# Kernel optimization log

Measured on AMD Instinct MI355X. Metric: run time of the kernel, lower is better.

Reference implementation:

```python
import jax, jax.numpy as jnp
import numpy as np

N, E, DIN, H, D = 100000, 1600000, 256, 4, 32  # nodes, edges, in_feats, heads, out_feats
NEG_SLOPE = 0.2


def setup_inputs() -> dict:
    key = jax.random.key(0)
    ks = jax.random.split(key, 6)
    feat = jax.random.normal(ks[0], (N, DIN), jnp.float32)
    src = jax.random.randint(ks[1], (E,), 0, N, jnp.int32)
    dst = jax.random.randint(ks[2], (E,), 0, N, jnp.int32)
    # fc weight, xavier-normal-ish scale
    W = jax.random.normal(ks[3], (H * D, DIN), jnp.float32) * (2.0 / (DIN + H * D)) ** 0.5
    attn_l = jax.random.normal(ks[4], (1, H, D), jnp.float32) * 0.1
    attn_r = jax.random.normal(ks[5], (1, H, D), jnp.float32) * 0.1
    bias = jnp.zeros((H * D,), jnp.float32)
    return dict(feat=feat, src=src, dst=dst, W=W, attn_l=attn_l, attn_r=attn_r, bias=bias)


def reference(feat, src, dst, W, attn_l, attn_r, bias):
    n = feat.shape[0]
    # node projection: [N, H, D]
    ft = (feat @ W.T).reshape(n, H, D)
    # per-node attention logits: [N, H]
    el = jnp.sum(ft * attn_l, axis=-1)
    er = jnp.sum(ft * attn_r, axis=-1)
    # edge scores (u_add_v + LeakyReLU): [E, H]
    e = jax.nn.leaky_relu(el[src] + er[dst], NEG_SLOPE)
    # segment softmax over incoming edges of each dst node
    m = jax.ops.segment_max(e, dst, num_segments=n)
    m = jnp.where(jnp.isfinite(m), m, 0.0)  # guard zero-in-degree nodes
    ae = jnp.exp(e - m[dst])
    denom = jax.ops.segment_sum(ae, dst, num_segments=n)
    a = ae / denom[dst]  # [E, H]
    # weighted scatter-aggregate (u_mul_e + sum): [N, H, D]
    out = jax.ops.segment_sum(ft[src] * a[:, :, None], dst, num_segments=n)
    return out + bias.reshape(1, H, D)
```

## Files before the change

### kernel.cpp

```cpp
#include <hip/hip_runtime.h>
#include <hip/hip_bf16.h>


#define DIN 256
#define HD 128
#define NEG_SLOPE 0.2f
#define BUCKW 1024
#define BINE 4096
#define CAP  18432

typedef float f32x4 __attribute__((ext_vector_type(4)));
typedef short s16x8 __attribute__((ext_vector_type(8)));

static __device__ __forceinline__ unsigned short f2bf(float x) {
    unsigned u = __float_as_uint(x);
    unsigned r = (u + 0x7FFFu + ((u >> 16) & 1u)) >> 16;
    return (unsigned short)r;
}
static __device__ __forceinline__ uint pk2(float a, float b) {
    return (uint)f2bf(a) | ((uint)f2bf(b) << 16);
}

__global__ __launch_bounds__(512, 4) void gemm_bin_kernel(
    const float* __restrict__ feat, const float* __restrict__ W,
    unsigned short* __restrict__ ftu, const float* __restrict__ attn_l,
    const float* __restrict__ attn_r, float* __restrict__ el,
    float* __restrict__ er, int n,
    const int* __restrict__ src, const int* __restrict__ dst,
    int* __restrict__ gcur, int* __restrict__ esrc,
    unsigned short* __restrict__ edlo, int e, int ngb)
{
    __shared__ unsigned short Bs[32768];
    const int tid = threadIdx.x;

    if ((int)blockIdx.x >= ngb) {
        int* h  = (int*)Bs;
        int* lb = h + 128;
        int* gb = lb + 128;
        int* sc = gb + 128;
        int* ptot = sc + 128;
        int* ps = ptot + 4;
        unsigned short* pd = (unsigned short*)(ps + BINE);
        unsigned char*  pb = (unsigned char*)(pd + BINE);
        if (tid < 128) h[tid] = 0;
        __syncthreads();
        const int base = ((int)blockIdx.x - ngb) * BINE + tid * 8;
        int sv[8], dv[8], rk[8];
        const int cnt = min(8, max(0, e - base));
        if (cnt == 8) {
            *(int4*)&sv[0] = *(const int4*)&src[base];
            *(int4*)&sv[4] = *(const int4*)&src[base + 4];
            *(int4*)&dv[0] = *(const int4*)&dst[base];
            *(int4*)&dv[4] = *(const int4*)&dst[base + 4];
        } else {
            for (int m = 0; m < cnt; ++m) { sv[m] = src[base + m]; dv[m] = dst[base + m]; }
        }
        for (int m = 0; m < cnt; ++m)
            rk[m] = atomicAdd(&h[dv[m] >> 10], 1);
        __syncthreads();
        if (tid < 128) sc[tid] = h[tid];
        __syncthreads();
        for (int off = 1; off < 128; off <<= 1) {
            int v = (tid < 128 && tid >= off) ? sc[tid - off] : 0;
            __syncthreads();
            if (tid < 128) sc[tid] += v;
            __syncthreads();
        }
        if (tid < 128) {
            lb[tid] = sc[tid] - h[tid];
            if (h[tid] > 0) gb[tid] = atomicAdd(&gcur[tid], h[tid]);
        }
        if (tid == 127) *ptot = sc[127];
        __syncthreads();
        for (int m = 0; m < cnt; ++m) {
            int b = dv[m] >> 10;
            int pos = lb[b] + rk[m];
            ps[pos] = sv[m];
            pd[pos] = (unsigned short)(dv[m] & 1023);
            pb[pos] = (unsigned char)b;
        }
        __syncthreads();
        const int tot = *ptot;
        for (int s = tid; s < tot; s += 512) {
            int b = pb[s];
            int o = b * CAP + gb[b] + (s - lb[b]);
            esrc[o] = ps[s];
            edlo[o] = pd[s];
        }
        return;
    }

    const int lane = tid & 63;
    const int wv = tid >> 6;
    const int l16 = lane & 15, lq = lane >> 4;
    const int row0 = (int)blockIdx.x * 256 + wv * 32;

#pragma unroll
    for (int it = 0; it < 8; ++it) {
        const int cell = it * 512 + tid;
        const int kb = cell >> 7, c = cell & 127;
        const float4* wp = (const float4*)&W[(size_t)c * DIN + kb * 8];
        float4 f0 = wp[0], f1 = wp[1];
        uint4 pk;
        pk.x = pk2(f0.x, f0.y); pk.y = pk2(f0.z, f0.w);
        pk.z = pk2(f1.x, f1.y); pk.w = pk2(f1.z, f1.w);
        *(uint4*)&Bs[(size_t)cell * 8] = pk;
    }
    __syncthreads();

    f32x4 acc[2][8] = {};
    const int ar0 = row0 + l16, ar1 = row0 + 16 + l16;
    const bool ok0 = ar0 < n, ok1 = ar1 < n;
    const float* fp0 = feat + (size_t)ar0 * DIN;
    const float* fp1 = feat + (size_t)ar1 * DIN;
#pragma unroll
    for (int kc = 0; kc < 4; ++kc) {
#pragma unroll
        for (int kk = 0; kk < 2; ++kk) {
            const int koff = kc * 64 + kk * 32 + lq * 8;
            union { s16x8 v; uint w[4]; } a0, a1;
            a0.v = (s16x8)(short)0;
            a1.v = (s16x8)(short)0;
            if (ok0) {
                float4 fa = *(const float4*)(fp0 + koff);
                float4 fb = *(const float4*)(fp0 + koff + 4);
                a0.w[0] = pk2(fa.x, fa.y); a0.w[1] = pk2(fa.z, fa.w);
                a0.w[2] = pk2(fb.x, fb.y); a0.w[3] = pk2(fb.z, fb.w);
            }
            if (ok1) {
                float4 fa = *(const float4*)(fp1 + koff);
                float4 fb = *(const float4*)(fp1 + koff + 4);
                a1.w[0] = pk2(fa.x, fa.y); a1.w[1] = pk2(fa.z, fa.w);
                a1.w[2] = pk2(fb.x, fb.y); a1.w[3] = pk2(fb.z, fb.w);
            }
            const int kb = kc * 8 + kk * 4 + lq;
#pragma unroll
            for (int n4 = 0; n4 < 8; ++n4) {
                s16x8 b = *(const s16x8*)&Bs[(kb * 128 + n4 * 16 + l16) * 8];
                acc[0][n4] = __builtin_amdgcn_mfma_f32_16x16x32_bf16(a0.v, b, acc[0][n4], 0, 0, 0);
                acc[1][n4] = __builtin_amdgcn_mfma_f32_16x16x32_bf16(a1.v, b, acc[1][n4], 0, 0, 0);
            }
        }
    }

    float al8[8], ar8[8];
#pragma unroll
    for (int n4 = 0; n4 < 8; ++n4) {
        al8[n4] = attn_l[n4 * 16 + l16];
        ar8[n4] = attn_r[n4 * 16 + l16];
    }
#pragma unroll
    for (int m = 0; m < 2; ++m) {
#pragma unroll
        for (int n4 = 0; n4 < 8; ++n4)
#pragma unroll
            for (int j = 0; j < 4; ++j) {
                int r = row0 + m * 16 + lq * 4 + j;
                if (r < n) ftu[(size_t)r * HD + n4 * 16 + l16] = f2bf(acc[m][n4][j]);
            }
#pragma unroll
        for (int j = 0; j < 4; ++j) {
            const int r = row0 + m * 16 + lq * 4 + j;
#pragma unroll
            for (int h = 0; h < 4; ++h) {
                float sl = acc[m][2 * h][j] * al8[2 * h] + acc[m][2 * h + 1][j] * al8[2 * h + 1];
                float sr = acc[m][2 * h][j] * ar8[2 * h] + acc[m][2 * h + 1][j] * ar8[2 * h + 1];
#pragma unroll
                for (int off = 1; off < 16; off <<= 1) {
                    sl += __shfl_xor(sl, off);
                    sr += __shfl_xor(sr, off);
                }
                if (l16 == ((j << 2) | h) && r < n) {
                    el[r * 4 + h] = sl;
                    er[r * 4 + h] = sr;
                }
            }
        }
    }
}

__global__ __launch_bounds__(1024) void fine_kernel(
    const int* __restrict__ esrc, const unsigned short* __restrict__ edlo,
    const int* __restrict__ gcur, int* __restrict__ beg, int* __restrict__ endp,
    int* __restrict__ srcs_sorted, int n)
{
    __shared__ int deg[1024];
    __shared__ int wsum[16];
    const int b = blockIdx.x, tid = threadIdx.x;
    const int lane = tid & 63, wid = tid >> 6;
    const int lo = b * CAP;
    const int cnt = gcur[b];
    const int nbase = b << 10;
    deg[tid] = 0;
    __syncthreads();
    for (int i = tid; i < cnt; i += 1024)
        atomicAdd(&deg[edlo[lo + i]], 1);
    __syncthreads();
    const int d = deg[tid];
    int x = d;
#pragma unroll
    for (int off = 1; off < 64; off <<= 1) {
        int y = __shfl(x, lane - off);
        if (lane >= off) x += y;
    }
    if (lane == 63) wsum[wid] = x;
    __syncthreads();
    if (tid == 0) {
        int run = 0;
#pragma unroll
        for (int i2 = 0; i2 < 16; ++i2) { int t2 = wsum[i2]; wsum[i2] = run; run += t2; }
    }
    __syncthreads();
    const int start = lo + wsum[wid] + x - d;
    if (nbase + tid < n) {
        beg[nbase + tid] = start;
        endp[nbase + tid] = start + d;
    }
    deg[tid] = start;
    __syncthreads();
    for (int i = tid; i < cnt; i += 1024) {
        int dd = edlo[lo + i];
        int pos = atomicAdd(&deg[dd], 1);
        srcs_sorted[pos] = esrc[lo + i];
    }
}

__global__ __launch_bounds__(256) void aggregate_kernel(
    const unsigned short* __restrict__ ftu, const float* __restrict__ el,
    const float* __restrict__ er, const int* __restrict__ beg,
    const int* __restrict__ endp, const int* __restrict__ srcs,
    const float* __restrict__ bias, float* __restrict__ out, int n)
{
    __shared__ float plds[4][64][4];
    int v = (int)((blockIdx.x * (unsigned)blockDim.x + threadIdx.x) >> 6);
    if (v >= n) return;
    const int wv = (threadIdx.x >> 6) & 3;
    const int lane = threadIdx.x & 63;
    const int h = lane >> 4;
    const int beg_ = beg[v], end_ = endp[v];
    const float4 er4 = *(const float4*)(er + (size_t)v * 4);
    const uint* __restrict__ ftu32 = (const uint*)ftu;
    float* pl = &plds[wv][0][0];
    float dn = 0.f;
    float acc0 = 0.f, acc1 = 0.f;
    for (int t = beg_; t < end_; t += 64) {
        const int cnt = min(64, end_ - t);
        int sj = 0;
        float p0 = 0.f, p1 = 0.f, p2 = 0.f, p3 = 0.f;
        if (lane < cnt) {
            sj = srcs[t + lane];
            float4 elv = *(const float4*)(el + (size_t)sj * 4);
            float e0 = elv.x + er4.x, e1 = elv.y + er4.y;
            float e2 = elv.z + er4.z, e3 = elv.w + er4.w;
            e0 = fmaxf(e0, NEG_SLOPE * e0);
            e1 = fmaxf(e1, NEG_SLOPE * e1);
            e2 = fmaxf(e2, NEG_SLOPE * e2);
            e3 = fmaxf(e3, NEG_SLOPE * e3);
            p0 = __expf(e0); p1 = __expf(e1);
            p2 = __expf(e2); p3 = __expf(e3);
        }
        *(float4*)&pl[lane << 2] = make_float4(p0, p1, p2, p3);
        __builtin_amdgcn_wave_barrier();
        for (int j = 0; j < cnt; j += 16) {
            uint u[16];
            float pj[16];
#pragma unroll
            for (int m = 0; m < 16; ++m) {
                int sjb = __shfl(sj, j + m);
                u[m] = ftu32[(uint)sjb * 64u + (uint)lane];
                pj[m] = pl[((j + m) << 2) + h];
            }
#pragma unroll
            for (int m = 0; m < 16; ++m) {
                dn += pj[m];
                acc0 = fmaf(pj[m], __uint_as_float(u[m] << 16), acc0);
                acc1 = fmaf(pj[m], __uint_as_float(u[m] & 0xffff0000u), acc1);
            }
        }
        __builtin_amdgcn_wave_barrier();
    }
    float inv = dn > 0.f ? 1.f / dn : 0.f;
    float b0 = bias[lane << 1], b1 = bias[(lane << 1) + 1];
    float2 o = make_float2(fmaf(acc0, inv, b0), fmaf(acc1, inv, b1));
    *(float2*)&out[(size_t)v * HD + (lane << 1)] = o;
}

extern "C" void kernel_launch(void* const* d_in, const int* in_sizes, int n_in,
                              void* d_out, int out_size, void* d_ws, size_t ws_size,
                              hipStream_t stream) {
    const float* feat   = (const float*)d_in[0];
    const int*   src    = (const int*)d_in[1];
    const int*   dst    = (const int*)d_in[2];
    const float* W      = (const float*)d_in[3];
    const float* attn_l = (const float*)d_in[4];
    const float* attn_r = (const float*)d_in[5];
    const float* bias   = (const float*)d_in[6];
    float* out = (float*)d_out;
    const int N = in_sizes[0] / DIN;
    const int E = in_sizes[1];
    const int NBUCK = (N + BUCKW - 1) / BUCKW;
    const int NGB = (N + 255) / 256;
    const int EB = (E + BINE - 1) / BINE;

    char* w = (char*)d_ws;
    auto alloc = [&](size_t bytes) {
        char* p = w;
        w += (bytes + 255) & ~(size_t)255;
        return p;
    };
    unsigned short* ftu         = (unsigned short*)alloc((size_t)N * HD * 2);
    float*          el          = (float*)alloc((size_t)N * 4 * 4);
    float*          er          = (float*)alloc((size_t)N * 4 * 4);
    int*            beg         = (int*)alloc((size_t)N * 4);
    int*            endp        = (int*)alloc((size_t)N * 4);
    int*            srcs_sorted = (int*)alloc((size_t)NBUCK * CAP * 4);
    int*            esrc        = (int*)alloc((size_t)NBUCK * CAP * 4);
    unsigned short* edlo        = (unsigned short*)alloc((size_t)NBUCK * CAP * 2);
    int*            gcur        = (int*)alloc(128 * 4);
    (void)ws_size;

    hipMemsetAsync(gcur, 0, 128 * 4, stream);
    gemm_bin_kernel<<<NGB + EB, 512, 0, stream>>>(
        feat, W, ftu, attn_l, attn_r, el, er, N,
        src, dst, gcur, esrc, edlo, E, NGB);
    fine_kernel<<<NBUCK, 1024, 0, stream>>>(esrc, edlo, gcur, beg, endp, srcs_sorted, N);
    aggregate_kernel<<<(N + 3) / 4, 256, 0, stream>>>(ftu, el, er, beg, endp, srcs_sorted, bias, out, N);
}
```

Measured before the change: 144.9 us.

## Retile projection GEMM to 128-row blocks with swizzled LDS A-tiles

The fused GEMM/binning kernel now uses 128-row tiles with a 4x2 wave grid, so each wave computes 32 rows by 64 columns instead of 32 rows by all 128 columns. The feature rows are staged through LDS with an XOR swizzle, and W is loaded in two K-halves, which shrinks the shared-memory footprint from 64KB to 48KB. The intent is to raise occupancy and spread the GEMM over more blocks. The cost is more barriers and extra LDS traffic for A, plus W is now reconverted by twice as many blocks.

```diff
diff --git a/kernel.cpp b/kernel.cpp
--- a/kernel.cpp
+++ b/kernel.cpp
@@ -8,6 +8,7 @@
 #define BUCKW 1024
 #define BINE 4096
 #define CAP  18432
+#define TM   128
 
 typedef float f32x4 __attribute__((ext_vector_type(4)));
 typedef short s16x8 __attribute__((ext_vector_type(8)));
@@ -30,11 +31,11 @@
     int* __restrict__ gcur, int* __restrict__ esrc,
     unsigned short* __restrict__ edlo, int e, int ngb)
 {
-    __shared__ unsigned short Bs[32768];
+    __shared__ unsigned short S[24576];
     const int tid = threadIdx.x;
 
     if ((int)blockIdx.x >= ngb) {
-        int* h  = (int*)Bs;
+        int* h  = (int*)S;
         int* lb = h + 128;
         int* gb = lb + 128;
         int* sc = gb + 128;
@@ -90,89 +91,96 @@
         return;
     }
 
+    unsigned short* Bsh = S;
+    unsigned short* As  = S + 16384;
     const int lane = tid & 63;
     const int wv = tid >> 6;
+    const int wr = wv >> 1, wc = wv & 1;
     const int l16 = lane & 15, lq = lane >> 4;
-    const int row0 = (int)blockIdx.x * 256 + wv * 32;
-
-#pragma unroll
-    for (int it = 0; it < 8; ++it) {
-        const int cell = it * 512 + tid;
-        const int kb = cell >> 7, c = cell & 127;
-        const float4* wp = (const float4*)&W[(size_t)c * DIN + kb * 8];
-        float4 f0 = wp[0], f1 = wp[1];
-        uint4 pk;
-        pk.x = pk2(f0.x, f0.y); pk.y = pk2(f0.z, f0.w);
-        pk.z = pk2(f1.x, f1.y); pk.w = pk2(f1.z, f1.w);
-        *(uint4*)&Bs[(size_t)cell * 8] = pk;
-    }
-    __syncthreads();
-
-    f32x4 acc[2][8] = {};
-    const int ar0 = row0 + l16, ar1 = row0 + 16 + l16;
-    const bool ok0 = ar0 < n, ok1 = ar1 < n;
-    const float* fp0 = feat + (size_t)ar0 * DIN;
-    const float* fp1 = feat + (size_t)ar1 * DIN;
-#pragma unroll
-    for (int kc = 0; kc < 4; ++kc) {
-#pragma unroll
-        for (int kk = 0; kk < 2; ++kk) {
-            const int koff = kc * 64 + kk * 32 + lq * 8;
-            union { s16x8 v; uint w[4]; } a0, a1;
-            a0.v = (s16x8)(short)0;
-            a1.v = (s16x8)(short)0;
-            if (ok0) {
-                float4 fa = *(const float4*)(fp0 + koff);
-                float4 fb = *(const float4*)(fp0 + koff + 4);
-                a0.w[0] = pk2(fa.x, fa.y); a0.w[1] = pk2(fa.z, fa.w);
-                a0.w[2] = pk2(fb.x, fb.y); a0.w[3] = pk2(fb.z, fb.w);
-            }
-            if (ok1) {
-                float4 fa = *(const float4*)(fp1 + koff);
-                float4 fb = *(const float4*)(fp1 + koff + 4);
-                a1.w[0] = pk2(fa.x, fa.y); a1.w[1] = pk2(fa.z, fa.w);
-                a1.w[2] = pk2(fb.x, fb.y); a1.w[3] = pk2(fb.z, fb.w);
-            }
-            const int kb = kc * 8 + kk * 4 + lq;
-#pragma unroll
-            for (int n4 = 0; n4 < 8; ++n4) {
-                s16x8 b = *(const s16x8*)&Bs[(kb * 128 + n4 * 16 + l16) * 8];
-                acc[0][n4] = __builtin_amdgcn_mfma_f32_16x16x32_bf16(a0.v, b, acc[0][n4], 0, 0, 0);
-                acc[1][n4] = __builtin_amdgcn_mfma_f32_16x16x32_bf16(a1.v, b, acc[1][n4], 0, 0, 0);
-            }
-        }
-    }
-
-    float al8[8], ar8[8];
-#pragma unroll
-    for (int n4 = 0; n4 < 8; ++n4) {
-        al8[n4] = attn_l[n4 * 16 + l16];
-        ar8[n4] = attn_r[n4 * 16 + l16];
+    const int row0 = (int)blockIdx.x * TM;
+
+    f32x4 acc[2][4] = {};
+
+    for (int p = 0; p < 2; ++p) {
+#pragma unroll
+        for (int it = 0; it < 4; ++it) {
+            const int cell = it * 512 + tid;
+            const int kbl = cell >> 7, c = cell & 127;
+            const float4* wp = (const float4*)&W[(size_t)c * DIN + (p * 16 + kbl) * 8];
+            float4 f0 = wp[0], f1 = wp[1];
+            uint4 pk;
+            pk.x = pk2(f0.x, f0.y); pk.y = pk2(f0.z, f0.w);
+            pk.z = pk2(f1.x, f1.y); pk.w = pk2(f1.z, f1.w);
+            *(uint4*)&Bsh[(size_t)cell * 8] = pk;
+        }
+#pragma unroll
+        for (int kc2 = 0; kc2 < 2; ++kc2) {
+            const int kc = p * 2 + kc2;
+#pragma unroll
+            for (int it = 0; it < 2; ++it) {
+                const int cell = it * 512 + tid;
+                const int r = cell >> 3, kq8 = (cell & 7) << 3;
+                uint4 pk = make_uint4(0, 0, 0, 0);
+                if (row0 + r < n) {
+                    const float4* ap = (const float4*)&feat[(size_t)(row0 + r) * DIN + kc * 64 + kq8];
+                    float4 f0 = ap[0], f1 = ap[1];
+                    pk.x = pk2(f0.x, f0.y); pk.y = pk2(f0.z, f0.w);
+                    pk.z = pk2(f1.x, f1.y); pk.w = pk2(f1.z, f1.w);
+                }
+                const int sidx = (r * 64 + kq8) ^ ((r & 7) << 3);
+                *(uint4*)&As[sidx] = pk;
+            }
+            __syncthreads();
+            const int ra = wr * 32 + l16;
+            const int swz = (ra & 7) << 3;
+#pragma unroll
+            for (int kk = 0; kk < 2; ++kk) {
+                const int kb8 = kk * 32 + lq * 8;
+                s16x8 a0 = *(const s16x8*)&As[(ra * 64 + kb8) ^ swz];
+                s16x8 a1 = *(const s16x8*)&As[((ra + 16) * 64 + kb8) ^ swz];
+                const int kbl = kc2 * 8 + kk * 4 + lq;
+#pragma unroll
+                for (int n4 = 0; n4 < 4; ++n4) {
+                    s16x8 b = *(const s16x8*)&Bsh[(kbl * 128 + wc * 64 + n4 * 16 + l16) * 8];
+                    acc[0][n4] = __builtin_amdgcn_mfma_f32_16x16x32_bf16(a0, b, acc[0][n4], 0, 0, 0);
+                    acc[1][n4] = __builtin_amdgcn_mfma_f32_16x16x32_bf16(a1, b, acc[1][n4], 0, 0, 0);
+                }
+            }
+            __syncthreads();
+        }
+    }
+
+    float al4[4], ar4[4];
+#pragma unroll
+    for (int n4 = 0; n4 < 4; ++n4) {
+        al4[n4] = attn_l[wc * 64 + n4 * 16 + l16];
+        ar4[n4] = attn_r[wc * 64 + n4 * 16 + l16];
     }
 #pragma unroll
     for (int m = 0; m < 2; ++m) {
 #pragma unroll
-        for (int n4 = 0; n4 < 8; ++n4)
+        for (int n4 = 0; n4 < 4; ++n4)
 #pragma unroll
             for (int j = 0; j < 4; ++j) {
-                int r = row0 + m * 16 + lq * 4 + j;
-                if (r < n) ftu[(size_t)r * HD + n4 * 16 + l16] = f2bf(acc[m][n4][j]);
+                int r = row0 + wr * 32 + m * 16 + lq * 4 + j;
+                if (r < n) ftu[(size_t)r * HD + wc * 64 + n4 * 16 + l16] = f2bf(acc[m][n4][j]);
             }
 #pragma unroll
         for (int j = 0; j < 4; ++j) {
-            const int r = row0 + m * 16 + lq * 4 + j;
-#pragma unroll
-            for (int h = 0; h < 4; ++h) {
-                float sl = acc[m][2 * h][j] * al8[2 * h] + acc[m][2 * h + 1][j] * al8[2 * h + 1];
-                float sr = acc[m][2 * h][j] * ar8[2 * h] + acc[m][2 * h + 1][j] * ar8[2 * h + 1];
+            const int r = row0 + wr * 32 + m * 16 + lq * 4 + j;
+#pragma unroll
+            for (int hh = 0; hh < 2; ++hh) {
+                float sl = acc[m][2 * hh][j] * al4[2 * hh] + acc[m][2 * hh + 1][j] * al4[2 * hh + 1];
+                float sr = acc[m][2 * hh][j] * ar4[2 * hh] + acc[m][2 * hh + 1][j] * ar4[2 * hh + 1];
 #pragma unroll
                 for (int off = 1; off < 16; off <<= 1) {
                     sl += __shfl_xor(sl, off);
                     sr += __shfl_xor(sr, off);
                 }
-                if (l16 == ((j << 2) | h) && r < n) {
-                    el[r * 4 + h] = sl;
-                    er[r * 4 + h] = sr;
+                if (l16 == ((j << 2) | (hh << 1)) && r < n) {
+                    const int gh = wc * 2 + hh;
+                    el[r * 4 + gh] = sl;
+                    er[r * 4 + gh] = sr;
                 }
             }
         }
@@ -299,7 +307,7 @@
     const int N = in_sizes[0] / DIN;
     const int E = in_sizes[1];
     const int NBUCK = (N + BUCKW - 1) / BUCKW;
-    const int NGB = (N + 255) / 256;
+    const int NGB = (N + TM - 1) / TM;
     const int EB = (E + BINE - 1) / BINE;
 
     char* w = (char*)d_ws;
```

New measurement: 157.4 us. 8.6% more time.

## Split fused GEMM/binning kernel and read pre-converted bf16 weights from global

Applied to the files above, without the earlier changes.

Undoes the fused launch that ran the projection GEMM and the edge binning as separate block roles inside one kernel. A small pre-pass now converts W to bf16 in the MFMA-friendly layout once. The GEMM kernel uses 256-thread blocks of 128 rows and reads B fragments straight from global/L2 rather than staging 64KB in LDS per block. The aim is to drop the redundant per-block W conversion and the large LDS footprint, which limits occupancy. The cost is two extra launches, and GEMM and binning now run one after the other instead of overlapping.

```diff
diff --git a/kernel.cpp b/kernel.cpp
--- a/kernel.cpp
+++ b/kernel.cpp
@@ -21,92 +21,24 @@
     return (uint)f2bf(a) | ((uint)f2bf(b) << 16);
 }
 
-__global__ __launch_bounds__(512, 4) void gemm_bin_kernel(
-    const float* __restrict__ feat, const float* __restrict__ W,
+__global__ void transw_kernel(const float* __restrict__ W, unsigned short* __restrict__ Wtb) {
+    int idx = blockIdx.x * blockDim.x + threadIdx.x;
+    if (idx >= HD * DIN) return;
+    int i = idx & 7, c = (idx >> 3) & 127, kb = idx >> 10;
+    Wtb[idx] = f2bf(W[(size_t)c * DIN + kb * 8 + i]);
+}
+
+__global__ __launch_bounds__(256, 4) void gemm_kernel(
+    const float* __restrict__ feat, const unsigned short* __restrict__ Wtb,
     unsigned short* __restrict__ ftu, const float* __restrict__ attn_l,
     const float* __restrict__ attn_r, float* __restrict__ el,
-    float* __restrict__ er, int n,
-    const int* __restrict__ src, const int* __restrict__ dst,
-    int* __restrict__ gcur, int* __restrict__ esrc,
-    unsigned short* __restrict__ edlo, int e, int ngb)
+    float* __restrict__ er, int n)
 {
-    __shared__ unsigned short Bs[32768];
     const int tid = threadIdx.x;
-
-    if ((int)blockIdx.x >= ngb) {
-        int* h  = (int*)Bs;
-        int* lb = h + 128;
-        int* gb = lb + 128;
-        int* sc = gb + 128;
-        int* ptot = sc + 128;
-        int* ps = ptot + 4;
-        unsigned short* pd = (unsigned short*)(ps + BINE);
-        unsigned char*  pb = (unsigned char*)(pd + BINE);
-        if (tid < 128) h[tid] = 0;
-        __syncthreads();
-        const int base = ((int)blockIdx.x - ngb) * BINE + tid * 8;
-        int sv[8], dv[8], rk[8];
-        const int cnt = min(8, max(0, e - base));
-        if (cnt == 8) {
-            *(int4*)&sv[0] = *(const int4*)&src[base];
-            *(int4*)&sv[4] = *(const int4*)&src[base + 4];
-            *(int4*)&dv[0] = *(const int4*)&dst[base];
-            *(int4*)&dv[4] = *(const int4*)&dst[base + 4];
-        } else {
-            for (int m = 0; m < cnt; ++m) { sv[m] = src[base + m]; dv[m] = dst[base + m]; }
-        }
-        for (int m = 0; m < cnt; ++m)
-            rk[m] = atomicAdd(&h[dv[m] >> 10], 1);
-        __syncthreads();
-        if (tid < 128) sc[tid] = h[tid];
-        __syncthreads();
-        for (int off = 1; off < 128; off <<= 1) {
-            int v = (tid < 128 && tid >= off) ? sc[tid - off] : 0;
-            __syncthreads();
-            if (tid < 128) sc[tid] += v;
-            __syncthreads();
-        }
-        if (tid < 128) {
-            lb[tid] = sc[tid] - h[tid];
-            if (h[tid] > 0) gb[tid] = atomicAdd(&gcur[tid], h[tid]);
-        }
-        if (tid == 127) *ptot = sc[127];
-        __syncthreads();
-        for (int m = 0; m < cnt; ++m) {
-            int b = dv[m] >> 10;
-            int pos = lb[b] + rk[m];
-            ps[pos] = sv[m];
-            pd[pos] = (unsigned short)(dv[m] & 1023);
-            pb[pos] = (unsigned char)b;
-        }
-        __syncthreads();
-        const int tot = *ptot;
-        for (int s = tid; s < tot; s += 512) {
-            int b = pb[s];
-            int o = b * CAP + gb[b] + (s - lb[b]);
-            esrc[o] = ps[s];
-            edlo[o] = pd[s];
-        }
-        return;
-    }
-
     const int lane = tid & 63;
     const int wv = tid >> 6;
     const int l16 = lane & 15, lq = lane >> 4;
-    const int row0 = (int)blockIdx.x * 256 + wv * 32;
-
-#pragma unroll
-    for (int it = 0; it < 8; ++it) {
-        const int cell = it * 512 + tid;
-        const int kb = cell >> 7, c = cell & 127;
-        const float4* wp = (const float4*)&W[(size_t)c * DIN + kb * 8];
-        float4 f0 = wp[0], f1 = wp[1];
-        uint4 pk;
-        pk.x = pk2(f0.x, f0.y); pk.y = pk2(f0.z, f0.w);
-        pk.z = pk2(f1.x, f1.y); pk.w = pk2(f1.z, f1.w);
-        *(uint4*)&Bs[(size_t)cell * 8] = pk;
-    }
-    __syncthreads();
+    const int row0 = (int)blockIdx.x * 128 + wv * 32;
 
     f32x4 acc[2][8] = {};
     const int ar0 = row0 + l16, ar1 = row0 + 16 + l16;
@@ -134,9 +66,10 @@
                 a1.w[2] = pk2(fb.x, fb.y); a1.w[3] = pk2(fb.z, fb.w);
             }
             const int kb = kc * 8 + kk * 4 + lq;
+            const unsigned short* bp = Wtb + ((size_t)kb * 128 + l16) * 8;
 #pragma unroll
             for (int n4 = 0; n4 < 8; ++n4) {
-                s16x8 b = *(const s16x8*)&Bs[(kb * 128 + n4 * 16 + l16) * 8];
+                s16x8 b = *(const s16x8*)(bp + n4 * 128);
                 acc[0][n4] = __builtin_amdgcn_mfma_f32_16x16x32_bf16(a0.v, b, acc[0][n4], 0, 0, 0);
                 acc[1][n4] = __builtin_amdgcn_mfma_f32_16x16x32_bf16(a1.v, b, acc[1][n4], 0, 0, 0);
             }
@@ -176,6 +109,63 @@
                 }
             }
         }
+    }
+}
+
+__global__ __launch_bounds__(512) void bin_kernel(
+    const int* __restrict__ src, const int* __restrict__ dst,
+    int* __restrict__ gcur, int* __restrict__ esrc,
+    unsigned short* __restrict__ edlo, int e)
+{
+    __shared__ int h[128], lb[128], gb[128], sc[128];
+    __shared__ int tot;
+    __shared__ int ps[BINE];
+    __shared__ unsigned short pd[BINE];
+    __shared__ unsigned char pb[BINE];
+    const int tid = threadIdx.x;
+    if (tid < 128) h[tid] = 0;
+    __syncthreads();
+    const int base = blockIdx.x * BINE + tid * 8;
+    int sv[8], dv[8], rk[8];
+    const int cnt = min(8, max(0, e - base));
+    if (cnt == 8) {
+        *(int4*)&sv[0] = *(const int4*)&src[base];
+        *(int4*)&sv[4] = *(const int4*)&src[base + 4];
+        *(int4*)&dv[0] = *(const int4*)&dst[base];
+        *(int4*)&dv[4] = *(const int4*)&dst[base + 4];
+    } else {
+        for (int m = 0; m < cnt; ++m) { sv[m] = src[base + m]; dv[m] = dst[base + m]; }
+    }
+    for (int m = 0; m < cnt; ++m)
+        rk[m] = atomicAdd(&h[dv[m] >> 10], 1);
+    __syncthreads();
+    if (tid < 128) sc[tid] = h[tid];
+    __syncthreads();
+    for (int off = 1; off < 128; off <<= 1) {
+        int v = (tid < 128 && tid >= off) ? sc[tid - off] : 0;
+        __syncthreads();
+        if (tid < 128) sc[tid] += v;
+        __syncthreads();
+    }
+    if (tid < 128) {
+        lb[tid] = sc[tid] - h[tid];
+        if (h[tid] > 0) gb[tid] = atomicAdd(&gcur[tid], h[tid]);
+    }
+    if (tid == 127) tot = sc[127];
+    __syncthreads();
+    for (int m = 0; m < cnt; ++m) {
+        int b = dv[m] >> 10;
+        int pos = lb[b] + rk[m];
+        ps[pos] = sv[m];
+        pd[pos] = (unsigned short)(dv[m] & 1023);
+        pb[pos] = (unsigned char)b;
+    }
+    __syncthreads();
+    for (int s = tid; s < tot; s += 512) {
+        int b = pb[s];
+        int o = b * CAP + gb[b] + (s - lb[b]);
+        esrc[o] = ps[s];
+        edlo[o] = pd[s];
     }
 }
 
@@ -299,7 +289,7 @@
     const int N = in_sizes[0] / DIN;
     const int E = in_sizes[1];
     const int NBUCK = (N + BUCKW - 1) / BUCKW;
-    const int NGB = (N + 255) / 256;
+    const int NGB = (N + 127) / 128;
     const int EB = (E + BINE - 1) / BINE;
 
     char* w = (char*)d_ws;
@@ -308,6 +298,7 @@
         w += (bytes + 255) & ~(size_t)255;
         return p;
     };
+    unsigned short* Wtb         = (unsigned short*)alloc((size_t)DIN * HD * 2);
     unsigned short* ftu         = (unsigned short*)alloc((size_t)N * HD * 2);
     float*          el          = (float*)alloc((size_t)N * 4 * 4);
     float*          er          = (float*)alloc((size_t)N * 4 * 4);
@@ -320,9 +311,9 @@
     (void)ws_size;
 
     hipMemsetAsync(gcur, 0, 128 * 4, stream);
-    gemm_bin_kernel<<<NGB + EB, 512, 0, stream>>>(
-        feat, W, ftu, attn_l, attn_r, el, er, N,
-        src, dst, gcur, esrc, edlo, E, NGB);
+    transw_kernel<<<(HD * DIN + 255) / 256, 256, 0, stream>>>(W, Wtb);
+    gemm_kernel<<<NGB, 256, 0, stream>>>(feat, Wtb, ftu, attn_l, attn_r, el, er, N);
+    bin_kernel<<<EB, 512, 0, stream>>>(src, dst, gcur, esrc, edlo, E);
     fine_kernel<<<NBUCK, 1024, 0, stream>>>(esrc, edlo, gcur, beg, endp, srcs_sorted, N);
     aggregate_kernel<<<(N + 3) / 4, 256, 0, stream>>>(ftu, el, er, beg, endp, srcs_sorted, bias, out, N);
 }
```

Result: slower. 166.4 us (+14.8%).
